# Performance work log

Measured on AMD Instinct MI355X. Metric: run time of the kernel, lower is better.

Reference implementation:

```python
import jax, jax.numpy as jnp
import numpy as np

N, C, H, O, NUM_CLASSES = 4096, 768, 512, 50, 1


def setup_inputs() -> dict:
    key = jax.random.key(0)
    ks = jax.random.split(key, 8)
    x = jax.random.normal(ks[0], (N, C), dtype=jnp.float32)
    labels = jax.random.randint(ks[1], (N,), 0, 2, dtype=jnp.int64)
    W1 = jax.random.normal(ks[2], (C, H), dtype=jnp.float32) / np.sqrt(C)
    b1 = jnp.zeros((H,), dtype=jnp.float32)
    W2 = jax.random.normal(ks[3], (H, O), dtype=jnp.float32) / np.sqrt(H)
    b2 = jnp.zeros((O,), dtype=jnp.float32)
    fcW = jax.random.normal(ks[4], (C + O, NUM_CLASSES), dtype=jnp.float32) / np.sqrt(C + O)
    fcb = jnp.zeros((NUM_CLASSES,), dtype=jnp.float32)
    return {"x": x, "labels": labels, "W1": W1, "b1": b1, "W2": W2, "b2": b2, "fcW": fcW, "fcb": fcb}


def _build_graph(x, labels):
    # similarity-threshold edge construction (dense masked form of the python double loop)
    sim = x @ x.T                                   # [N, N]
    n = x.shape[0]
    diff = labels[:, None] != labels[None, :]       # cross-label pairs
    cnt = jnp.sum(diff)
    s = jnp.sum(jnp.where(diff, sim, 0.0))
    threshold = jnp.where(cnt > 0, s / cnt.astype(sim.dtype), jnp.asarray(0.0, sim.dtype))
    eye = jnp.eye(n, dtype=bool)
    same = (labels[:, None] == labels[None, :]) & ~eye
    edge_mask = same & (sim <= threshold)           # symmetric (sim symmetric)
    loss_mask = edge_mask & (jnp.arange(n)[:, None] < jnp.arange(n)[None, :])  # i<j pairs
    adj = jax.lax.stop_gradient(edge_mask.astype(x.dtype))
    # GCN normalization with self-loops
    a = adj + jnp.eye(n, dtype=x.dtype)
    dinv = jax.lax.rsqrt(jnp.sum(a, axis=1))        # deg >= 1
    norm_adj = dinv[:, None] * a * dinv[None, :]
    return norm_adj, loss_mask


def reference(x, labels, W1, b1, W2, b2, fcW, fcb):
    norm_adj, loss_mask = _build_graph(x, labels)
    h = jax.nn.relu(norm_adj @ (x @ W1) + b1)       # conv1 + relu
    g = norm_adj @ (h @ W2) + b2                    # conv2
    f_g = jnp.concatenate([x, g], axis=-1)          # [N, C+O]
    out = f_g @ fcW + fcb                           # [N, 1]
    return out, f_g, loss_mask, x
```

## Files before the change

### kernel.cpp

```cpp
#include <hip/hip_runtime.h>
#include <hip/hip_bf16.h>
#include <math.h>

#define NN 4096
#define CD 768
#define HD 512
#define OD 50
#define FGD 818

typedef short short8 __attribute__((ext_vector_type(8)));
typedef _Float16 half8 __attribute__((ext_vector_type(8)));
typedef float f32x4 __attribute__((ext_vector_type(4)));
typedef unsigned short us4 __attribute__((ext_vector_type(4)));
typedef unsigned short ushortT;
typedef unsigned char uchar;
typedef unsigned long long u64;

__device__ inline ushortT f2bf(float v) {
    __hip_bfloat16 b = __float2bfloat16(v);
    return *(ushortT*)&b;
}
__device__ inline float bf2f(ushortT u) {
    __hip_bfloat16 b = *(__hip_bfloat16*)&u;
    return __bfloat162float(b);
}
__device__ inline float dinv_of(int d) {
    return (float)(1.0 / sqrt((double)(1 + d)));
}

__global__ __launch_bounds__(256) void gdot_kernel(const double* __restrict__ gsum,
                                                   const int* __restrict__ labels,
                                                   double* __restrict__ scal) {
    int t = threadIdx.x;
    double d = 0.0;
    for (int c = t; c < CD; c += 256) d += gsum[c] * gsum[768 + c];
    int n0 = 0;
    for (int i = t; i < NN; i += 256) n0 += (labels[i] == 0) ? 1 : 0;
    for (int off = 32; off; off >>= 1) {
        d += __shfl_down(d, off);
        n0 += __shfl_down(n0, off);
    }
    __shared__ double sd[4];
    __shared__ int sn[4];
    int wid = t >> 6, lane = t & 63;
    if (lane == 0) { sd[wid] = d; sn[wid] = n0; }
    __syncthreads();
    if (t == 0) {
        double D = sd[0] + sd[1] + sd[2] + sd[3];
        double N0 = (double)(sn[0] + sn[1] + sn[2] + sn[3]);
        scal[0] = 2.0 * D;
        scal[1] = 2.0 * N0 * ((double)NN - N0);
    }
}

#define BAND 0.10
#define RC_CAP (1 << 18)
#define RCB 256

__global__ __launch_bounds__(256) void simk4(
    const ushortT* __restrict__ xf, const ushortT* __restrict__ xh,
    const ushortT* __restrict__ w1t, const int* __restrict__ labels,
    const double* __restrict__ scal, u64* __restrict__ abbits,
    float* __restrict__ lm, int* __restrict__ deg,
    int* __restrict__ rc_cnt, int* __restrict__ rc_list,
    float* __restrict__ xw1f) {
    __shared__ ushortT lds[2 * 64 * 72];
    __shared__ int larr[128];
    __shared__ int rcbuf[RCB];
    __shared__ int rcn, rcbase;
    int tid = threadIdx.x;
    int lane = tid & 63;
    int w = tid >> 6;
    int wr = w >> 1, wc = w & 1;
    int m = lane & 15, quad = lane >> 4;

    if (blockIdx.x >= 2080) {
        int idx = blockIdx.x - 2080;
        int row0 = (idx >> 3) * 64, col0 = (idx & 7) * 64;
        f32x4 acc[2][2] = {{{0.f, 0.f, 0.f, 0.f}, {0.f, 0.f, 0.f, 0.f}},
                           {{0.f, 0.f, 0.f, 0.f}, {0.f, 0.f, 0.f, 0.f}}};
        for (int k0 = 0; k0 < CD; k0 += 64) {
#pragma unroll
            for (int t = 0; t < 2; ++t) {
                int id2 = tid + t * 256;
                int row = id2 >> 3, c8 = (id2 & 7) * 8;
                *(short8*)&lds[row * 72 + c8] =
                    *(const short8*)&xh[(size_t)(row0 + row) * CD + k0 + c8];
                *(short8*)&lds[4608 + row * 72 + c8] =
                    *(const short8*)&w1t[(size_t)(col0 + row) * CD + k0 + c8];
            }
            __syncthreads();
#pragma unroll
            for (int ks = 0; ks < 2; ++ks) {
                short8 af[2], bf[2];
#pragma unroll
                for (int i = 0; i < 2; ++i)
                    af[i] = *(const short8*)&lds[(wr * 32 + i * 16 + m) * 72 +
                                                 ks * 32 + quad * 8];
#pragma unroll
                for (int j = 0; j < 2; ++j)
                    bf[j] = *(const short8*)&lds[4608 +
                                                 (wc * 32 + j * 16 + m) * 72 +
                                                 ks * 32 + quad * 8];
#pragma unroll
                for (int i = 0; i < 2; ++i)
#pragma unroll
                    for (int j = 0; j < 2; ++j)
                        acc[i][j] = __builtin_amdgcn_mfma_f32_16x16x32_bf16(
                            af[i], bf[j], acc[i][j], 0, 0, 0);
            }
            __syncthreads();
        }
#pragma unroll
        for (int i = 0; i < 2; ++i)
#pragma unroll
            for (int j = 0; j < 2; ++j) {
                int row = row0 + wr * 32 + i * 16 + quad * 4;
                int col = col0 + wc * 32 + j * 16 + m;
                *(f32x4*)&xw1f[(size_t)col * NN + row] = acc[i][j];
            }
        return;
    }

    int bid = blockIdx.x;
    int sid = (bid & 7) * 260 + (bid >> 3);
    int sby = 0, rem = sid;
    for (; sby < 8; ++sby) {
        int rowsz = 36 + (7 - sby) * 64;
        if (rem < rowsz) break;
        rem -= rowsz;
    }
    int sbx, iby, ibx;
    if (rem < 36) {
        sbx = sby;
        iby = 0;
        while (rem >= 8 - iby) { rem -= 8 - iby; ++iby; }
        ibx = iby + rem;
    } else {
        rem -= 36;
        sbx = sby + 1 + (rem >> 6);
        int u = rem & 63;
        iby = u >> 3; ibx = u & 7;
    }
    int by = sby * 8 + iby, bx = sbx * 8 + ibx;
    bool diag = (bx == by);
    int row0 = by * 64, col0 = bx * 64;

    if (tid == 0) rcn = 0;
    if (tid < 64) larr[tid] = labels[row0 + tid];
    else if (tid < 128) larr[tid] = labels[col0 + tid - 64];

    f32x4 acc[2][2] = {{{0.f, 0.f, 0.f, 0.f}, {0.f, 0.f, 0.f, 0.f}},
                       {{0.f, 0.f, 0.f, 0.f}, {0.f, 0.f, 0.f, 0.f}}};

    const size_t rowbase = (size_t)row0 * CD;
    const size_t colbase = (size_t)col0 * CD;
    short8 rg[2][2];
#pragma unroll
    for (int tt = 0; tt < 2; ++tt) {
        int id2 = tid + tt * 256;
        int row = id2 >> 3, c8 = (id2 & 7) * 8;
        rg[tt][0] = *(const short8*)&xf[rowbase + (size_t)row * CD + c8];
        rg[tt][1] = *(const short8*)&xf[colbase + (size_t)row * CD + c8];
    }

    for (int k0 = 0; k0 < CD; k0 += 64) {
        __syncthreads();
#pragma unroll
        for (int tt = 0; tt < 2; ++tt) {
            int id2 = tid + tt * 256;
            int row = id2 >> 3, c8 = (id2 & 7) * 8;
            *(short8*)&lds[0 * 4608 + row * 72 + c8] = rg[tt][0];
            *(short8*)&lds[1 * 4608 + row * 72 + c8] = rg[tt][1];
        }
        __syncthreads();
        if (k0 + 64 < CD) {
#pragma unroll
            for (int tt = 0; tt < 2; ++tt) {
                int id2 = tid + tt * 256;
                int row = id2 >> 3, c8 = (id2 & 7) * 8 + k0 + 64;
                rg[tt][0] = *(const short8*)&xf[rowbase + (size_t)row * CD + c8];
                rg[tt][1] = *(const short8*)&xf[colbase + (size_t)row * CD + c8];
            }
        }
#pragma unroll
        for (int ks = 0; ks < 2; ++ks) {
            half8 ah[2], bh[2];
#pragma unroll
            for (int i = 0; i < 2; ++i)
                ah[i] = *(const half8*)&lds[(wr * 32 + i * 16 + m) * 72 +
                                            ks * 32 + quad * 8];
#pragma unroll
            for (int j = 0; j < 2; ++j)
                bh[j] = *(const half8*)&lds[4608 + (wc * 32 + j * 16 + m) * 72 +
                                            ks * 32 + quad * 8];
#pragma unroll
            for (int i = 0; i < 2; ++i)
#pragma unroll
                for (int j = 0; j < 2; ++j)
                    acc[i][j] = __builtin_amdgcn_mfma_f32_16x16x32_f16(
                        ah[i], bh[j], acc[i][j], 0, 0, 0);
        }
    }
    __syncthreads();

    double thrd;
    {
        double cnt = scal[1];
        thrd = (cnt > 0.0) ? (scal[0] / cnt) : 0.0;
    }
    uchar* flags = (uchar*)lds;
#pragma unroll
    for (int i = 0; i < 2; ++i)
#pragma unroll
        for (int j = 0; j < 2; ++j) {
#pragma unroll
            for (int r = 0; r < 4; ++r) {
                int row = wr * 32 + i * 16 + quad * 4 + r;
                int col = wc * 32 + j * 16 + m;
                bool same = (larr[row] == larr[64 + col]);
                bool selfp = ((row0 + row) == (col0 + col));
                bool edge = false;
                if (same && !selfp) {
                    double s = (double)acc[i][j][r];
                    if (s <= thrd - BAND) {
                        edge = true;
                    } else if (s <= thrd + BAND) {
                        edge = (s <= thrd);
                        int enc = ((row0 + row) << 12) | (col0 + col) |
                                  (diag ? 0 : (1 << 24)) |
                                  (edge ? (1 << 25) : 0);
                        int slot = atomicAdd(&rcn, 1);
                        if (slot < RCB) rcbuf[slot] = enc;
                    }
                }
                flags[row * 68 + col] = edge ? 1 : 0;
            }
        }
    __syncthreads();
    if (tid == 0) {
        int n = rcn < RCB ? rcn : RCB;
        rcbase = n ? atomicAdd(rc_cnt, n) : 0;
    }

    {
        int r = tid >> 2, q = tid & 3;
        int cnti = 0;
        unsigned int bits16 = 0;
#pragma unroll
        for (int s = 0; s < 4; ++s) {
            int cb = q * 16 + s * 4;
            float4 f;
#pragma unroll
            for (int k2 = 0; k2 < 4; ++k2) {
                int c = cb + k2;
                bool fl = flags[r * 68 + c] != 0;
                cnti += fl ? 1 : 0;
                if (fl || (diag && r == c)) bits16 |= 1u << (s * 4 + k2);
                ((float*)&f)[k2] = (fl && (row0 + r < col0 + c)) ? 1.0f : 0.0f;
            }
            *(float4*)&lm[(size_t)(row0 + r) * NN + col0 + cb] = f;
        }
        unsigned int s1 = __shfl_down(bits16, 1);
        unsigned int s2 = __shfl_down(bits16, 2);
        unsigned int s3 = __shfl_down(bits16, 3);
        cnti += __shfl_down(cnti, 1);
        cnti += __shfl_down(cnti, 2);
        if (q == 0) {
            u64 u = (u64)bits16 | ((u64)s1 << 16) | ((u64)s2 << 32) |
                    ((u64)s3 << 48);
            abbits[(size_t)(row0 + r) * 64 + bx] = u;
            if (cnti) atomicAdd(&deg[row0 + r], cnti);
        }
    }

    if (!diag) {
        int c = tid >> 2, q = tid & 3;
        int cnti = 0;
        unsigned int bits16 = 0;
        float4 fz = {0.0f, 0.0f, 0.0f, 0.0f};
#pragma unroll
        for (int s = 0; s < 4; ++s) {
            int rb = q * 16 + s * 4;
#pragma unroll
            for (int k2 = 0; k2 < 4; ++k2) {
                bool fl = flags[(rb + k2) * 68 + c] != 0;
                cnti += fl ? 1 : 0;
                if (fl) bits16 |= 1u << (s * 4 + k2);
            }
            *(float4*)&lm[(size_t)(col0 + c) * NN + row0 + rb] = fz;
        }
        unsigned int s1 = __shfl_down(bits16, 1);
        unsigned int s2 = __shfl_down(bits16, 2);
        unsigned int s3 = __shfl_down(bits16, 3);
        cnti += __shfl_down(cnti, 1);
        cnti += __shfl_down(cnti, 2);
        if (q == 0) {
            u64 u = (u64)bits16 | ((u64)s1 << 16) | ((u64)s2 << 32) |
                    ((u64)s3 << 48);
            abbits[(size_t)(col0 + c) * 64 + by] = u;
            if (cnti) atomicAdd(&deg[col0 + c], cnti);
        }
    }

    __syncthreads();
    {
        int n = rcn < RCB ? rcn : RCB;
        if (tid < n) {
            int idx = rcbase + tid;
            if (idx < RC_CAP) rc_list[idx] = rcbuf[tid];
        }
    }
}

__global__ __launch_bounds__(256) void rc_fix(
    const float* __restrict__ x, const double* __restrict__ scal,
    const int* __restrict__ rc_cnt, const int* __restrict__ rc_list,
    u64* __restrict__ abbits, float* __restrict__ lm, int* __restrict__ deg) {
    int cnt = *rc_cnt;
    if (cnt > RC_CAP) cnt = RC_CAP;
    double thrd;
    {
        double c = scal[1];
        thrd = (c > 0.0) ? (scal[0] / c) : 0.0;
    }
    int lane = threadIdx.x & 63;
    int wid = (blockIdx.x * 256 + threadIdx.x) >> 6;
    int nw = (gridDim.x * 256) >> 6;
    for (int e = wid; e < cnt; e += nw) {
        int enc = rc_list[e];
        int c = enc & 0xFFF;
        int r = (enc >> 12) & 0xFFF;
        bool mirror = (enc >> 24) & 1;
        bool prov = (enc >> 25) & 1;
        const float* xi = x + (size_t)r * CD;
        const float* xj = x + (size_t)c * CD;
        double d = 0.0;
#pragma unroll
        for (int s = 0; s < 12; ++s)
            d += (double)xi[lane + s * 64] * (double)xj[lane + s * 64];
        for (int off = 32; off; off >>= 1) d += __shfl_down(d, off);
        if (lane == 0) {
            bool exact = (d <= thrd);
            if (exact != prov) {
                u64 mk = 1ull << (c & 63);
                if (exact) atomicOr(&abbits[(size_t)r * 64 + (c >> 6)], mk);
                else       atomicAnd(&abbits[(size_t)r * 64 + (c >> 6)], ~mk);
                lm[(size_t)r * NN + c] = (exact && r < c) ? 1.0f : 0.0f;
                int dlt = exact ? 1 : -1;
                atomicAdd(&deg[r], dlt);
                if (mirror) {
                    u64 mk2 = 1ull << (r & 63);
                    if (exact) atomicOr(&abbits[(size_t)c * 64 + (r >> 6)], mk2);
                    else       atomicAnd(&abbits[(size_t)c * 64 + (r >> 6)], ~mk2);
                    atomicAdd(&deg[c], dlt);
                }
            }
        }
    }
}

__global__ __launch_bounds__(256) void scaleT(const float* __restrict__ xw1f,
                                              const int* __restrict__ deg,
                                              ushortT* __restrict__ xw1sT) {
    size_t i = ((size_t)blockIdx.x * 256 + threadIdx.x) * 4;
    float4 v = *(const float4*)&xw1f[i];
    int r = (int)(i & (NN - 1));
    us4 o;
    o[0] = f2bf(v.x / sqrtf((float)(1 + deg[r])));
    o[1] = f2bf(v.y / sqrtf((float)(1 + deg[r + 1])));
    o[2] = f2bf(v.z / sqrtf((float)(1 + deg[r + 2])));
    o[3] = f2bf(v.w / sqrtf((float)(1 + deg[r + 3])));
    *(us4*)&xw1sT[i] = o;
}

__global__ __launch_bounds__(256) void prep_kernel(
    const float* __restrict__ x, const float* __restrict__ W1,
    const float* __restrict__ W2, const int* __restrict__ labels,
    float* __restrict__ fg, float* __restrict__ xo,
    ushortT* __restrict__ xh, ushortT* __restrict__ xf, ushortT* __restrict__ w1t,
    ushortT* __restrict__ w2t, double* __restrict__ gsum) {
    int b = blockIdx.x;
    if (b < 4096) {
        int t = threadIdx.x;
        if (t < 192) {
            float4 v = *(const float4*)&x[(size_t)b * CD + t * 4];
            *(float4*)&xo[(size_t)b * CD + t * 4] = v;
            fg[(size_t)b * FGD + t * 4 + 0] = v.x;
            fg[(size_t)b * FGD + t * 4 + 1] = v.y;
            fg[(size_t)b * FGD + t * 4 + 2] = v.z;
            fg[(size_t)b * FGD + t * 4 + 3] = v.w;
            us4 hh, ff;
            float* vp = (float*)&v;
#pragma unroll
            for (int k = 0; k < 4; ++k) {
                ((ushortT*)&hh)[k] = f2bf(vp[k]);
                _Float16 g = (_Float16)vp[k];
                ((ushortT*)&ff)[k] = *(ushortT*)&g;
            }
            *(us4*)&xh[(size_t)b * CD + t * 4] = hh;
            *(us4*)&xf[(size_t)b * CD + t * 4] = ff;
        }
        return;
    }
    if (b >= 4512) {
        int bb = b - 4512;
        int t = threadIdx.x;
        double a0[3] = {0, 0, 0}, a1[3] = {0, 0, 0};
        for (int rr = 0; rr < 16; ++rr) {
            int row = bb * 16 + rr;
            int lab = labels[row];
#pragma unroll
            for (int s = 0; s < 3; ++s) {
                double v = (double)x[(size_t)row * CD + t + s * 256];
                if (lab == 0) a0[s] += v; else a1[s] += v;
            }
        }
#pragma unroll
        for (int s = 0; s < 3; ++s) {
            atomicAdd(&gsum[t + s * 256], a0[s]);
            atomicAdd(&gsum[768 + t + s * 256], a1[s]);
        }
        return;
    }
    __shared__ float tT[32][33];
    const float* P;
    ushortT* T;
    int K, N, Npad, k0, n0;
    if (b < 4480) {
        int bb = b - 4096;
        P = W1; T = w1t; K = CD; N = HD; Npad = HD;
        k0 = (bb % 24) * 32; n0 = (bb / 24) * 32;
    } else {
        int bb = b - 4480;
        P = W2; T = w2t; K = HD; N = OD; Npad = 64;
        k0 = (bb % 16) * 32; n0 = (bb / 16) * 32;
    }
    int tx = threadIdx.x & 31, ty = threadIdx.x >> 5;
#pragma unroll
    for (int s = 0; s < 4; ++s) {
        int k = k0 + ty + s * 8, n = n0 + tx;
        tT[ty + s * 8][tx] = (k < K && n < N) ? P[(size_t)k * N + n] : 0.0f;
    }
    __syncthreads();
#pragma unroll
    for (int s = 0; s < 4; ++s) {
        int n = n0 + ty + s * 8, k = k0 + tx;
        if (n < Npad && k < K) T[(size_t)n * K + k] = f2bf(tT[tx][ty + s * 8]);
    }
}

__global__ __launch_bounds__(256) void gemm_part(
    const ushortT* __restrict__ A, const ushortT* __restrict__ B,
    float* __restrict__ P, int M, int K, int KC) {
    __shared__ ushortT lds[2 * 64 * 72];
    int tid = threadIdx.x;
    int lane = tid & 63;
    int w = tid >> 6;
    int wr = w >> 1, wc = w & 1;
    int m = lane & 15, quad = lane >> 4;
    int kb = blockIdx.x;
    int row0 = blockIdx.y * 64;
    int kbase = kb * KC;

    f32x4 acc[2][2] = {{{0.f, 0.f, 0.f, 0.f}, {0.f, 0.f, 0.f, 0.f}},
                       {{0.f, 0.f, 0.f, 0.f}, {0.f, 0.f, 0.f, 0.f}}};

    for (int k0 = 0; k0 < KC; k0 += 64) {
#pragma unroll
        for (int t = 0; t < 2; ++t) {
            int id2 = tid + t * 256;
            int row = id2 >> 3, c8 = (id2 & 7) * 8;
            *(short8*)&lds[row * 72 + c8] =
                *(const short8*)&A[(size_t)(row0 + row) * K + kbase + k0 + c8];
            *(short8*)&lds[4608 + row * 72 + c8] =
                *(const short8*)&B[(size_t)row * K + kbase + k0 + c8];
        }
        __syncthreads();
#pragma unroll
        for (int ks = 0; ks < 2; ++ks) {
            short8 af[2], bf[2];
#pragma unroll
            for (int i = 0; i < 2; ++i)
                af[i] = *(const short8*)&lds[(wr * 32 + i * 16 + m) * 72 +
                                             ks * 32 + quad * 8];
#pragma unroll
            for (int j = 0; j < 2; ++j)
                bf[j] = *(const short8*)&lds[4608 + (wc * 32 + j * 16 + m) * 72 +
                                             ks * 32 + quad * 8];
#pragma unroll
            for (int i = 0; i < 2; ++i)
#pragma unroll
                for (int j = 0; j < 2; ++j)
                    acc[i][j] = __builtin_amdgcn_mfma_f32_16x16x32_bf16(
                        af[i], bf[j], acc[i][j], 0, 0, 0);
        }
        __syncthreads();
    }
#pragma unroll
    for (int i = 0; i < 2; ++i)
#pragma unroll
        for (int j = 0; j < 2; ++j)
#pragma unroll
            for (int r = 0; r < 4; ++r) {
                int row = wr * 32 + i * 16 + quad * 4 + r;
                int col = wc * 32 + j * 16 + m;
                P[((size_t)kb * M + row0 + row) * 64 + col] = acc[i][j][r];
            }
}

__global__ __launch_bounds__(256) void gemm_partB(
    const u64* __restrict__ Abits, const ushortT* __restrict__ B,
    float* __restrict__ P, int M, int K, int KC) {
    __shared__ ushortT lds[2 * 64 * 72];
    int tid = threadIdx.x;
    int lane = tid & 63;
    int w = tid >> 6;
    int wr = w >> 1, wc = w & 1;
    int m = lane & 15, quad = lane >> 4;
    int kb = blockIdx.x;
    int row0 = blockIdx.y * 64;
    int kbase = kb * KC;
    int er = tid >> 2, eq = tid & 3;

    f32x4 acc[2][2] = {{{0.f, 0.f, 0.f, 0.f}, {0.f, 0.f, 0.f, 0.f}},
                       {{0.f, 0.f, 0.f, 0.f}, {0.f, 0.f, 0.f, 0.f}}};

    for (int k0 = 0; k0 < KC; k0 += 64) {
#pragma unroll
        for (int t = 0; t < 2; ++t) {
            int id2 = tid + t * 256;
            int row = id2 >> 3, c8 = (id2 & 7) * 8;
            *(short8*)&lds[4608 + row * 72 + c8] =
                *(const short8*)&B[(size_t)row * K + kbase + k0 + c8];
        }
        {
            u64 bits = Abits[(size_t)(row0 + er) * 64 + ((kbase + k0) >> 6)];
            unsigned int half = (unsigned int)(bits >> (eq * 16)) & 0xFFFFu;
            short8 v0, v1;
#pragma unroll
            for (int k = 0; k < 8; ++k) {
                ((ushortT*)&v0)[k] =
                    ((half >> k) & 1) ? (ushortT)0x3F80 : (ushortT)0;
                ((ushortT*)&v1)[k] =
                    ((half >> (k + 8)) & 1) ? (ushortT)0x3F80 : (ushortT)0;
            }
            *(short8*)&lds[er * 72 + eq * 16] = v0;
            *(short8*)&lds[er * 72 + eq * 16 + 8] = v1;
        }
        __syncthreads();
#pragma unroll
        for (int ks = 0; ks < 2; ++ks) {
            short8 af[2], bf[2];
#pragma unroll
            for (int i = 0; i < 2; ++i)
                af[i] = *(const short8*)&lds[(wr * 32 + i * 16 + m) * 72 +
                                             ks * 32 + quad * 8];
#pragma unroll
            for (int j = 0; j < 2; ++j)
                bf[j] = *(const short8*)&lds[4608 + (wc * 32 + j * 16 + m) * 72 +
                                             ks * 32 + quad * 8];
#pragma unroll
            for (int i = 0; i < 2; ++i)
#pragma unroll
                for (int j = 0; j < 2; ++j)
                    acc[i][j] = __builtin_amdgcn_mfma_f32_16x16x32_bf16(
                        af[i], bf[j], acc[i][j], 0, 0, 0);
        }
        __syncthreads();
    }
#pragma unroll
    for (int i = 0; i < 2; ++i)
#pragma unroll
        for (int j = 0; j < 2; ++j)
#pragma unroll
            for (int r = 0; r < 4; ++r) {
                int row = wr * 32 + i * 16 + quad * 4 + r;
                int col = wc * 32 + j * 16 + m;
                P[((size_t)kb * M + row0 + row) * 64 + col] = acc[i][j][r];
            }
}

__global__ __launch_bounds__(256) void gemm_partWB(
    const u64* __restrict__ Abits, const ushortT* __restrict__ B,
    float* __restrict__ P, int M, int K, int KC, int ldP) {
    __shared__ ushortT lds[2 * 64 * 72];
    int tid = threadIdx.x;
    int lane = tid & 63;
    int w = tid >> 6;
    int wr = w >> 1, wc = w & 1;
    int m = lane & 15, quad = lane >> 4;
    int col0 = blockIdx.x * 64;
    int row0 = blockIdx.y * 64;
    int kb = blockIdx.z;
    int kbase = kb * KC;
    int er = tid >> 2, eq = tid & 3;

    f32x4 acc[2][2] = {{{0.f, 0.f, 0.f, 0.f}, {0.f, 0.f, 0.f, 0.f}},
                       {{0.f, 0.f, 0.f, 0.f}, {0.f, 0.f, 0.f, 0.f}}};

    for (int k0 = 0; k0 < KC; k0 += 64) {
#pragma unroll
        for (int t = 0; t < 2; ++t) {
            int id2 = tid + t * 256;
            int row = id2 >> 3, c8 = (id2 & 7) * 8;
            *(short8*)&lds[4608 + row * 72 + c8] =
                *(const short8*)&B[(size_t)(col0 + row) * K + kbase + k0 + c8];
        }
        {
            u64 bits = Abits[(size_t)(row0 + er) * 64 + ((kbase + k0) >> 6)];
            unsigned int half = (unsigned int)(bits >> (eq * 16)) & 0xFFFFu;
            short8 v0, v1;
#pragma unroll
            for (int k = 0; k < 8; ++k) {
                ((ushortT*)&v0)[k] =
                    ((half >> k) & 1) ? (ushortT)0x3F80 : (ushortT)0;
                ((ushortT*)&v1)[k] =
                    ((half >> (k + 8)) & 1) ? (ushortT)0x3F80 : (ushortT)0;
            }
            *(short8*)&lds[er * 72 + eq * 16] = v0;
            *(short8*)&lds[er * 72 + eq * 16 + 8] = v1;
        }
        __syncthreads();
#pragma unroll
        for (int ks = 0; ks < 2; ++ks) {
            short8 af[2], bf[2];
#pragma unroll
            for (int i = 0; i < 2; ++i)
                af[i] = *(const short8*)&lds[(wr * 32 + i * 16 + m) * 72 +
                                             ks * 32 + quad * 8];
#pragma unroll
            for (int j = 0; j < 2; ++j)
                bf[j] = *(const short8*)&lds[4608 + (wc * 32 + j * 16 + m) * 72 +
                                             ks * 32 + quad * 8];
#pragma unroll
            for (int i = 0; i < 2; ++i)
#pragma unroll
                for (int j = 0; j < 2; ++j)
                    acc[i][j] = __builtin_amdgcn_mfma_f32_16x16x32_bf16(
                        af[i], bf[j], acc[i][j], 0, 0, 0);
        }
        __syncthreads();
    }
#pragma unroll
    for (int i = 0; i < 2; ++i)
#pragma unroll
        for (int j = 0; j < 2; ++j)
#pragma unroll
            for (int r = 0; r < 4; ++r) {
                int row = wr * 32 + i * 16 + quad * 4 + r;
                int col = wc * 32 + j * 16 + m;
                P[((size_t)kb * M + row0 + row) * ldP + col0 + col] =
                    acc[i][j][r];
            }
}

__global__ __launch_bounds__(256) void k5_epi(const float* __restrict__ P5,
                                              const int* __restrict__ deg,
                                              const float* __restrict__ b1,
                                              ushortT* __restrict__ hb) {
    int tid = threadIdx.x;
    int cg = tid & 127;
    int rr = tid >> 7;
#pragma unroll
    for (int p = 0; p < 2; ++p) {
        int r = blockIdx.x * 4 + p * 2 + rr;
        float dv = dinv_of(deg[r]);
        float4 s = {0.f, 0.f, 0.f, 0.f};
#pragma unroll
        for (int kb = 0; kb < 4; ++kb) {
            float4 v = *(const float4*)&P5[((size_t)kb * NN + r) * HD + cg * 4];
            s.x += v.x; s.y += v.y; s.z += v.z; s.w += v.w;
        }
        float4 bv = *(const float4*)&b1[cg * 4];
        us4 o;
        o[0] = f2bf(fmaxf(s.x * dv + bv.x, 0.f));
        o[1] = f2bf(fmaxf(s.y * dv + bv.y, 0.f));
        o[2] = f2bf(fmaxf(s.z * dv + bv.z, 0.f));
        o[3] = f2bf(fmaxf(s.w * dv + bv.w, 0.f));
        *(us4*)&hb[(size_t)r * HD + cg * 4] = o;
    }
}

__global__ __launch_bounds__(256) void k6_epi(const float* __restrict__ P6,
                                              const int* __restrict__ deg,
                                              ushortT* __restrict__ hw2sT) {
    __shared__ ushortT Th[64 * 72];
    int row0 = blockIdx.x * 64;
    int tid = threadIdx.x;
    int rl = tid >> 2, q = tid & 3;
    float dv = dinv_of(deg[row0 + rl]);
#pragma unroll
    for (int s = 0; s < 16; ++s) {
        int c = q * 16 + s;
        float v = 0.f;
#pragma unroll
        for (int kb = 0; kb < 8; ++kb)
            v += P6[((size_t)kb * NN + row0 + rl) * 64 + c];
        Th[c * 72 + rl] = f2bf(v * dv);
    }
    __syncthreads();
#pragma unroll
    for (int t = 0; t < 2; ++t) {
        int id2 = tid + t * 256;
        int cc = id2 >> 3, chunk = id2 & 7;
        *(short8*)&hw2sT[(size_t)cc * NN + row0 + chunk * 8] =
            *(const short8*)&Th[cc * 72 + chunk * 8];
    }
}

__global__ __launch_bounds__(256) void k7_epi_out(
    const float* __restrict__ P7, const int* __restrict__ deg,
    const float* __restrict__ b2, const float* __restrict__ fcW,
    const float* __restrict__ fcb, float* __restrict__ fg,
    float* __restrict__ out) {
    int row0 = blockIdx.x * 64;
    int tid = threadIdx.x;
    int rl = tid >> 2, q = tid & 3;
    int r = row0 + rl;
    float dv = dinv_of(deg[r]);
    float sg = 0.f;
#pragma unroll
    for (int s = 0; s < 16; ++s) {
        int c = q * 16 + s;
        if (c < OD) {
            float v = 0.f;
#pragma unroll
            for (int kb = 0; kb < 16; ++kb)
                v += P7[((size_t)kb * NN + r) * 64 + c];
            v = v * dv + b2[c];
            fg[(size_t)r * FGD + CD + c] = v;
            sg += v * fcW[CD + c];
        }
    }
    const float* fr = fg + (size_t)r * FGD;
    float sx = 0.f;
    for (int k = q * 192; k < (q + 1) * 192; k += 2) {
        float2 vv = *(const float2*)&fr[k];
        float2 ww = *(const float2*)&fcW[k];
        sx += vv.x * ww.x + vv.y * ww.y;
    }
    float s = sx + sg;
    s += __shfl_down(s, 1);
    s += __shfl_down(s, 2);
    if (q == 0) out[r] = s + fcb[0];
}

extern "C" void kernel_launch(void* const* d_in, const int* in_sizes, int n_in,
                              void* d_out, int out_size, void* d_ws, size_t ws_size,
                              hipStream_t stream) {
    const float* x = (const float*)d_in[0];
    const int* labels = (const int*)d_in[1];
    const float* W1 = (const float*)d_in[2];
    const float* b1 = (const float*)d_in[3];
    const float* W2 = (const float*)d_in[4];
    const float* b2 = (const float*)d_in[5];
    const float* fcW = (const float*)d_in[6];
    const float* fcb = (const float*)d_in[7];
    float* outp = (float*)d_out;

    const size_t o_out = 0;
    const size_t o_fg = 4096;
    const size_t o_lm = o_fg + (size_t)NN * FGD;
    const size_t o_x = o_lm + (size_t)NN * NN;

    char* ws = (char*)d_ws;
    size_t off = 0;
    u64* abbits = (u64*)(ws + off); off += (size_t)NN * 64 * 8;
    ushortT* xh = (ushortT*)(ws + off); off += (size_t)NN * CD * 2;
    ushortT* xf = (ushortT*)(ws + off); off += (size_t)NN * CD * 2;
    ushortT* w1t = (ushortT*)(ws + off); off += (size_t)HD * CD * 2;
    ushortT* xw1sT = (ushortT*)(ws + off); off += (size_t)HD * NN * 2;
    ushortT* hb = (ushortT*)(ws + off); off += (size_t)NN * HD * 2;
    ushortT* w2t = (ushortT*)(ws + off); off += (size_t)64 * HD * 2;
    ushortT* hw2sT = (ushortT*)(ws + off); off += (size_t)64 * NN * 2;
    char* zbase = ws + off;
    int* deg = (int*)(ws + off); off += (size_t)NN * 4;
    double* gsum = (double*)(ws + off); off += 1536 * 8;
    double* scal = (double*)(ws + off); off += 16;
    int* rc_cnt = (int*)(ws + off); off += 16;
    size_t zbytes = (size_t)NN * 4 + 1536 * 8 + 16 + 16;
    char* uni = ws + off;
    int* rc_list = (int*)uni;
    float* xw1f = (float*)(uni + (1 << 20));
    float* P5 = (float*)uni;
    float* P6 = (float*)uni;
    float* P7 = (float*)uni;
    off += (size_t)4 * NN * HD * 4;

    hipMemsetAsync(zbase, 0, zbytes, stream);

    prep_kernel<<<4768, 256, 0, stream>>>(x, W1, W2, labels, outp + o_fg,
                                          outp + o_x, xh, xf, w1t, w2t, gsum);

    gdot_kernel<<<1, 256, 0, stream>>>(gsum, labels, scal);

    simk4<<<2592, 256, 0, stream>>>(xf, xh, w1t, labels, scal, abbits,
                                    outp + o_lm, deg, rc_cnt, rc_list, xw1f);

    rc_fix<<<512, 256, 0, stream>>>(x, scal, rc_cnt, rc_list, abbits, outp + o_lm,
                                    deg);

    scaleT<<<(HD * NN / 4) / 256, 256, 0, stream>>>(xw1f, deg, xw1sT);

    gemm_partWB<<<dim3(HD / 64, NN / 64, 4), 256, 0, stream>>>(
        abbits, xw1sT, P5, NN, NN, NN / 4, HD);
    k5_epi<<<NN / 4, 256, 0, stream>>>(P5, deg, b1, hb);

    gemm_part<<<dim3(8, NN / 64), 256, 0, stream>>>(hb, w2t, P6, NN, HD, HD / 8);
    k6_epi<<<NN / 64, 256, 0, stream>>>(P6, deg, hw2sT);

    gemm_partB<<<dim3(16, NN / 64), 256, 0, stream>>>(abbits, hw2sT, P7, NN, NN,
                                                      NN / 16);
    k7_epi_out<<<NN / 64, 256, 0, stream>>>(P7, deg, b2, fcW, fcb, outp + o_fg,
                                            outp + o_out);
}
```

Baseline: 306.8 us.

## Use async global-to-LDS double buffering in sim GEMM and fuse degree scaling into gemm

The similarity GEMM in simk4 now uses global_load_lds direct-to-LDS loads into a double-buffered, XOR-swizzled LDS layout, so the next K tile is fetched while the current one is computed. This replaces the register-staged prefetch and removes one barrier per iteration. Separately, the scaleT kernel is removed: gemm_partWB now reads the fp32 XW1 directly, scales it by the per-row dinv values, and converts to bf16 while loading tiles. That saves a launch and an intermediate write and read, but doubles the bytes the B operand loads and adds conversion work inside the GEMM.

New measurement: 315.8 us. 2.9% more time.

```diff
diff --git a/kernel.cpp b/kernel.cpp
--- a/kernel.cpp
+++ b/kernel.cpp
@@ -26,6 +26,11 @@
 }
 __device__ inline float dinv_of(int d) {
     return (float)(1.0 / sqrt((double)(1 + d)));
+}
+__device__ inline void gload16(const void* g, void* l) {
+    __builtin_amdgcn_global_load_lds(
+        (const __attribute__((address_space(1))) void*)g,
+        (__attribute__((address_space(3))) void*)l, 16, 0, 0);
 }
 
 __global__ __launch_bounds__(256) void gdot_kernel(const double* __restrict__ gsum,
@@ -64,7 +69,7 @@
     float* __restrict__ lm, int* __restrict__ deg,
     int* __restrict__ rc_cnt, int* __restrict__ rc_list,
     float* __restrict__ xw1f) {
-    __shared__ ushortT lds[2 * 64 * 72];
+    __shared__ ushortT lds2[16384];
     __shared__ int larr[128];
     __shared__ int rcbuf[RCB];
     __shared__ int rcn, rcbase;
@@ -84,9 +89,9 @@
             for (int t = 0; t < 2; ++t) {
                 int id2 = tid + t * 256;
                 int row = id2 >> 3, c8 = (id2 & 7) * 8;
-                *(short8*)&lds[row * 72 + c8] =
+                *(short8*)&lds2[row * 72 + c8] =
                     *(const short8*)&xh[(size_t)(row0 + row) * CD + k0 + c8];
-                *(short8*)&lds[4608 + row * 72 + c8] =
+                *(short8*)&lds2[4608 + row * 72 + c8] =
                     *(const short8*)&w1t[(size_t)(col0 + row) * CD + k0 + c8];
             }
             __syncthreads();
@@ -95,13 +100,13 @@
                 short8 af[2], bf[2];
 #pragma unroll
                 for (int i = 0; i < 2; ++i)
-                    af[i] = *(const short8*)&lds[(wr * 32 + i * 16 + m) * 72 +
-                                                 ks * 32 + quad * 8];
+                    af[i] = *(const short8*)&lds2[(wr * 32 + i * 16 + m) * 72 +
+                                                  ks * 32 + quad * 8];
 #pragma unroll
                 for (int j = 0; j < 2; ++j)
-                    bf[j] = *(const short8*)&lds[4608 +
-                                                 (wc * 32 + j * 16 + m) * 72 +
-                                                 ks * 32 + quad * 8];
+                    bf[j] = *(const short8*)&lds2[4608 +
+                                                  (wc * 32 + j * 16 + m) * 72 +
+                                                  ks * 32 + quad * 8];
 #pragma unroll
                 for (int i = 0; i < 2; ++i)
 #pragma unroll
@@ -155,45 +160,45 @@
 
     const size_t rowbase = (size_t)row0 * CD;
     const size_t colbase = (size_t)col0 * CD;
-    short8 rg[2][2];
-#pragma unroll
-    for (int tt = 0; tt < 2; ++tt) {
-        int id2 = tid + tt * 256;
-        int row = id2 >> 3, c8 = (id2 & 7) * 8;
-        rg[tt][0] = *(const short8*)&xf[rowbase + (size_t)row * CD + c8];
-        rg[tt][1] = *(const short8*)&xf[colbase + (size_t)row * CD + c8];
-    }
-
-    for (int k0 = 0; k0 < CD; k0 += 64) {
-        __syncthreads();
-#pragma unroll
-        for (int tt = 0; tt < 2; ++tt) {
-            int id2 = tid + tt * 256;
-            int row = id2 >> 3, c8 = (id2 & 7) * 8;
-            *(short8*)&lds[0 * 4608 + row * 72 + c8] = rg[tt][0];
-            *(short8*)&lds[1 * 4608 + row * 72 + c8] = rg[tt][1];
-        }
-        __syncthreads();
-        if (k0 + 64 < CD) {
-#pragma unroll
-            for (int tt = 0; tt < 2; ++tt) {
-                int id2 = tid + tt * 256;
-                int row = id2 >> 3, c8 = (id2 & 7) * 8 + k0 + 64;
-                rg[tt][0] = *(const short8*)&xf[rowbase + (size_t)row * CD + c8];
-                rg[tt][1] = *(const short8*)&xf[colbase + (size_t)row * CD + c8];
-            }
-        }
+    int p = w >> 1;
+    const ushortT* src = xf + (p ? colbase : rowbase);
+    int gsub = (w & 1) * 4;
+    int lrow = lane >> 3, lchunk = lane & 7;
+    int cc = lchunk ^ lrow;
+
+    auto stage = [&](int buf, int k0) {
+#pragma unroll
+        for (int i = 0; i < 4; ++i) {
+            int g = gsub + i;
+            int grow = g * 8 + lrow;
+            const void* gp = (const void*)(src + (size_t)grow * CD + k0 + cc * 8);
+            int loff = buf * 16384 + p * 8192 + g * 1024;
+            loff = __builtin_amdgcn_readfirstlane(loff);
+            gload16(gp, (char*)lds2 + loff);
+        }
+    };
+
+    stage(0, 0);
+    __syncthreads();
+    int cur = 0;
+    for (int t = 0; t < CD / 64; ++t) {
+        if (t < CD / 64 - 1) stage(cur ^ 1, (t + 1) * 64);
 #pragma unroll
         for (int ks = 0; ks < 2; ++ks) {
             half8 ah[2], bh[2];
-#pragma unroll
-            for (int i = 0; i < 2; ++i)
-                ah[i] = *(const half8*)&lds[(wr * 32 + i * 16 + m) * 72 +
-                                            ks * 32 + quad * 8];
-#pragma unroll
-            for (int j = 0; j < 2; ++j)
-                bh[j] = *(const half8*)&lds[4608 + (wc * 32 + j * 16 + m) * 72 +
-                                            ks * 32 + quad * 8];
+            int jj = ks * 4 + quad;
+#pragma unroll
+            for (int i = 0; i < 2; ++i) {
+                int row = wr * 32 + i * 16 + m;
+                ah[i] = *(const half8*)&lds2[cur * 8192 + row * 64 +
+                                             ((jj ^ (row & 7)) << 3)];
+            }
+#pragma unroll
+            for (int j = 0; j < 2; ++j) {
+                int row = wc * 32 + j * 16 + m;
+                bh[j] = *(const half8*)&lds2[cur * 8192 + 4096 + row * 64 +
+                                             ((jj ^ (row & 7)) << 3)];
+            }
 #pragma unroll
             for (int i = 0; i < 2; ++i)
 #pragma unroll
@@ -201,15 +206,16 @@
                     acc[i][j] = __builtin_amdgcn_mfma_f32_16x16x32_f16(
                         ah[i], bh[j], acc[i][j], 0, 0, 0);
         }
-    }
-    __syncthreads();
+        __syncthreads();
+        cur ^= 1;
+    }
 
     double thrd;
     {
         double cnt = scal[1];
         thrd = (cnt > 0.0) ? (scal[0] / cnt) : 0.0;
     }
-    uchar* flags = (uchar*)lds;
+    uchar* flags = (uchar*)lds2;
 #pragma unroll
     for (int i = 0; i < 2; ++i)
 #pragma unroll
@@ -360,20 +366,6 @@
     }
 }
 
-__global__ __launch_bounds__(256) void scaleT(const float* __restrict__ xw1f,
-                                              const int* __restrict__ deg,
-                                              ushortT* __restrict__ xw1sT) {
-    size_t i = ((size_t)blockIdx.x * 256 + threadIdx.x) * 4;
-    float4 v = *(const float4*)&xw1f[i];
-    int r = (int)(i & (NN - 1));
-    us4 o;
-    o[0] = f2bf(v.x / sqrtf((float)(1 + deg[r])));
-    o[1] = f2bf(v.y / sqrtf((float)(1 + deg[r + 1])));
-    o[2] = f2bf(v.z / sqrtf((float)(1 + deg[r + 2])));
-    o[3] = f2bf(v.w / sqrtf((float)(1 + deg[r + 3])));
-    *(us4*)&xw1sT[i] = o;
-}
-
 __global__ __launch_bounds__(256) void prep_kernel(
     const float* __restrict__ x, const float* __restrict__ W1,
     const float* __restrict__ W2, const int* __restrict__ labels,
@@ -582,9 +574,11 @@
 }
 
 __global__ __launch_bounds__(256) void gemm_partWB(
-    const u64* __restrict__ Abits, const ushortT* __restrict__ B,
-    float* __restrict__ P, int M, int K, int KC, int ldP) {
+    const u64* __restrict__ Abits, const float* __restrict__ Bf,
+    const int* __restrict__ deg, float* __restrict__ P,
+    int M, int K, int KC, int ldP) {
     __shared__ ushortT lds[2 * 64 * 72];
+    __shared__ float dinvK[1024];
     int tid = threadIdx.x;
     int lane = tid & 63;
     int w = tid >> 6;
@@ -596,6 +590,10 @@
     int kbase = kb * KC;
     int er = tid >> 2, eq = tid & 3;
 
+    for (int v = tid; v < KC; v += 256)
+        dinvK[v] = 1.0f / sqrtf((float)(1 + deg[kbase + v]));
+    __syncthreads();
+
     f32x4 acc[2][2] = {{{0.f, 0.f, 0.f, 0.f}, {0.f, 0.f, 0.f, 0.f}},
                        {{0.f, 0.f, 0.f, 0.f}, {0.f, 0.f, 0.f, 0.f}}};
 
@@ -604,8 +602,19 @@
         for (int t = 0; t < 2; ++t) {
             int id2 = tid + t * 256;
             int row = id2 >> 3, c8 = (id2 & 7) * 8;
-            *(short8*)&lds[4608 + row * 72 + c8] =
-                *(const short8*)&B[(size_t)(col0 + row) * K + kbase + k0 + c8];
+            const float* bp = &Bf[(size_t)(col0 + row) * K + kbase + k0 + c8];
+            float4 v0 = *(const float4*)bp;
+            float4 v1 = *(const float4*)(bp + 4);
+            short8 o;
+            ((ushortT*)&o)[0] = f2bf(v0.x * dinvK[k0 + c8 + 0]);
+            ((ushortT*)&o)[1] = f2bf(v0.y * dinvK[k0 + c8 + 1]);
+            ((ushortT*)&o)[2] = f2bf(v0.z * dinvK[k0 + c8 + 2]);
+            ((ushortT*)&o)[3] = f2bf(v0.w * dinvK[k0 + c8 + 3]);
+            ((ushortT*)&o)[4] = f2bf(v1.x * dinvK[k0 + c8 + 4]);
+            ((ushortT*)&o)[5] = f2bf(v1.y * dinvK[k0 + c8 + 5]);
+            ((ushortT*)&o)[6] = f2bf(v1.z * dinvK[k0 + c8 + 6]);
+            ((ushortT*)&o)[7] = f2bf(v1.w * dinvK[k0 + c8 + 7]);
+            *(short8*)&lds[4608 + row * 72 + c8] = o;
         }
         {
             u64 bits = Abits[(size_t)(row0 + er) * 64 + ((kbase + k0) >> 6)];
@@ -770,7 +779,7 @@
     ushortT* xh = (ushortT*)(ws + off); off += (size_t)NN * CD * 2;
     ushortT* xf = (ushortT*)(ws + off); off += (size_t)NN * CD * 2;
     ushortT* w1t = (ushortT*)(ws + off); off += (size_t)HD * CD * 2;
-    ushortT* xw1sT = (ushortT*)(ws + off); off += (size_t)HD * NN * 2;
+    float* xw1f = (float*)(ws + off); off += (size_t)HD * NN * 4;
     ushortT* hb = (ushortT*)(ws + off); off += (size_t)NN * HD * 2;
     ushortT* w2t = (ushortT*)(ws + off); off += (size_t)64 * HD * 2;
     ushortT* hw2sT = (ushortT*)(ws + off); off += (size_t)64 * NN * 2;
@@ -782,7 +791,6 @@
     size_t zbytes = (size_t)NN * 4 + 1536 * 8 + 16 + 16;
     char* uni = ws + off;
     int* rc_list = (int*)uni;
-    float* xw1f = (float*)(uni + (1 << 20));
     float* P5 = (float*)uni;
     float* P6 = (float*)uni;
     float* P7 = (float*)uni;
@@ -801,10 +809,8 @@
     rc_fix<<<512, 256, 0, stream>>>(x, scal, rc_cnt, rc_list, abbits, outp + o_lm,
                                     deg);
 
-    scaleT<<<(HD * NN / 4) / 256, 256, 0, stream>>>(xw1f, deg, xw1sT);
-
     gemm_partWB<<<dim3(HD / 64, NN / 64, 4), 256, 0, stream>>>(
-        abbits, xw1sT, P5, NN, NN, NN / 4, HD);
+        abbits, xw1f, deg, P5, NN, NN, NN / 4, HD);
     k5_epi<<<NN / 4, 256, 0, stream>>>(P5, deg, b1, hb);
 
     gemm_part<<<dim3(8, NN / 64), 256, 0, stream>>>(hb, w2t, P6, NN, HD, HD / 8);
```

## Fuse degree scaling into GEMM B-load and fold h@W2 into conv1 epilogue

Applied to the files above, without the earlier changes.

Removes the scaleT kernel by having gemm_partWB read the fp32 X·W1 buffer directly, scale it by per-k D^-1/2 (cached in shared memory) and convert it to bf16 while staging into LDS. It also merges k5_epi, the h@W2 GEMM and k6_epi into one k56_epi kernel. That kernel keeps 4 rows of relu(h) in shared memory and computes the 64-column product with scalar FMAs. This cuts three launches and the hb/P6 round trips through memory. The cost is that the big GEMM now reads fp32 B, twice the bytes, and the small GEMM runs on plain ALUs instead of MFMA.

New measurement: 325.3 us. +6.0%, slower.

```diff
diff --git a/kernel.cpp b/kernel.cpp
--- a/kernel.cpp
+++ b/kernel.cpp
@@ -360,20 +360,6 @@
     }
 }
 
-__global__ __launch_bounds__(256) void scaleT(const float* __restrict__ xw1f,
-                                              const int* __restrict__ deg,
-                                              ushortT* __restrict__ xw1sT) {
-    size_t i = ((size_t)blockIdx.x * 256 + threadIdx.x) * 4;
-    float4 v = *(const float4*)&xw1f[i];
-    int r = (int)(i & (NN - 1));
-    us4 o;
-    o[0] = f2bf(v.x / sqrtf((float)(1 + deg[r])));
-    o[1] = f2bf(v.y / sqrtf((float)(1 + deg[r + 1])));
-    o[2] = f2bf(v.z / sqrtf((float)(1 + deg[r + 2])));
-    o[3] = f2bf(v.w / sqrtf((float)(1 + deg[r + 3])));
-    *(us4*)&xw1sT[i] = o;
-}
-
 __global__ __launch_bounds__(256) void prep_kernel(
     const float* __restrict__ x, const float* __restrict__ W1,
     const float* __restrict__ W2, const int* __restrict__ labels,
@@ -450,65 +436,6 @@
     }
 }
 
-__global__ __launch_bounds__(256) void gemm_part(
-    const ushortT* __restrict__ A, const ushortT* __restrict__ B,
-    float* __restrict__ P, int M, int K, int KC) {
-    __shared__ ushortT lds[2 * 64 * 72];
-    int tid = threadIdx.x;
-    int lane = tid & 63;
-    int w = tid >> 6;
-    int wr = w >> 1, wc = w & 1;
-    int m = lane & 15, quad = lane >> 4;
-    int kb = blockIdx.x;
-    int row0 = blockIdx.y * 64;
-    int kbase = kb * KC;
-
-    f32x4 acc[2][2] = {{{0.f, 0.f, 0.f, 0.f}, {0.f, 0.f, 0.f, 0.f}},
-                       {{0.f, 0.f, 0.f, 0.f}, {0.f, 0.f, 0.f, 0.f}}};
-
-    for (int k0 = 0; k0 < KC; k0 += 64) {
-#pragma unroll
-        for (int t = 0; t < 2; ++t) {
-            int id2 = tid + t * 256;
-            int row = id2 >> 3, c8 = (id2 & 7) * 8;
-            *(short8*)&lds[row * 72 + c8] =
-                *(const short8*)&A[(size_t)(row0 + row) * K + kbase + k0 + c8];
-            *(short8*)&lds[4608 + row * 72 + c8] =
-                *(const short8*)&B[(size_t)row * K + kbase + k0 + c8];
-        }
-        __syncthreads();
-#pragma unroll
-        for (int ks = 0; ks < 2; ++ks) {
-            short8 af[2], bf[2];
-#pragma unroll
-            for (int i = 0; i < 2; ++i)
-                af[i] = *(const short8*)&lds[(wr * 32 + i * 16 + m) * 72 +
-                                             ks * 32 + quad * 8];
-#pragma unroll
-            for (int j = 0; j < 2; ++j)
-                bf[j] = *(const short8*)&lds[4608 + (wc * 32 + j * 16 + m) * 72 +
-                                             ks * 32 + quad * 8];
-#pragma unroll
-            for (int i = 0; i < 2; ++i)
-#pragma unroll
-                for (int j = 0; j < 2; ++j)
-                    acc[i][j] = __builtin_amdgcn_mfma_f32_16x16x32_bf16(
-                        af[i], bf[j], acc[i][j], 0, 0, 0);
-        }
-        __syncthreads();
-    }
-#pragma unroll
-    for (int i = 0; i < 2; ++i)
-#pragma unroll
-        for (int j = 0; j < 2; ++j)
-#pragma unroll
-            for (int r = 0; r < 4; ++r) {
-                int row = wr * 32 + i * 16 + quad * 4 + r;
-                int col = wc * 32 + j * 16 + m;
-                P[((size_t)kb * M + row0 + row) * 64 + col] = acc[i][j][r];
-            }
-}
-
 __global__ __launch_bounds__(256) void gemm_partB(
     const u64* __restrict__ Abits, const ushortT* __restrict__ B,
     float* __restrict__ P, int M, int K, int KC) {
@@ -582,9 +509,11 @@
 }
 
 __global__ __launch_bounds__(256) void gemm_partWB(
-    const u64* __restrict__ Abits, const ushortT* __restrict__ B,
-    float* __restrict__ P, int M, int K, int KC, int ldP) {
+    const u64* __restrict__ Abits, const float* __restrict__ Bf,
+    const int* __restrict__ deg, float* __restrict__ P,
+    int M, int K, int KC, int ldP) {
     __shared__ ushortT lds[2 * 64 * 72];
+    __shared__ float dinvK[1024];
     int tid = threadIdx.x;
     int lane = tid & 63;
     int w = tid >> 6;
@@ -596,6 +525,10 @@
     int kbase = kb * KC;
     int er = tid >> 2, eq = tid & 3;
 
+    for (int v = tid; v < KC; v += 256)
+        dinvK[v] = 1.0f / sqrtf((float)(1 + deg[kbase + v]));
+    __syncthreads();
+
     f32x4 acc[2][2] = {{{0.f, 0.f, 0.f, 0.f}, {0.f, 0.f, 0.f, 0.f}},
                        {{0.f, 0.f, 0.f, 0.f}, {0.f, 0.f, 0.f, 0.f}}};
 
@@ -604,8 +537,19 @@
         for (int t = 0; t < 2; ++t) {
             int id2 = tid + t * 256;
             int row = id2 >> 3, c8 = (id2 & 7) * 8;
-            *(short8*)&lds[4608 + row * 72 + c8] =
-                *(const short8*)&B[(size_t)(col0 + row) * K + kbase + k0 + c8];
+            const float* bp = &Bf[(size_t)(col0 + row) * K + kbase + k0 + c8];
+            float4 v0 = *(const float4*)bp;
+            float4 v1 = *(const float4*)(bp + 4);
+            short8 o;
+            ((ushortT*)&o)[0] = f2bf(v0.x * dinvK[k0 + c8 + 0]);
+            ((ushortT*)&o)[1] = f2bf(v0.y * dinvK[k0 + c8 + 1]);
+            ((ushortT*)&o)[2] = f2bf(v0.z * dinvK[k0 + c8 + 2]);
+            ((ushortT*)&o)[3] = f2bf(v0.w * dinvK[k0 + c8 + 3]);
+            ((ushortT*)&o)[4] = f2bf(v1.x * dinvK[k0 + c8 + 4]);
+            ((ushortT*)&o)[5] = f2bf(v1.y * dinvK[k0 + c8 + 5]);
+            ((ushortT*)&o)[6] = f2bf(v1.z * dinvK[k0 + c8 + 6]);
+            ((ushortT*)&o)[7] = f2bf(v1.w * dinvK[k0 + c8 + 7]);
+            *(short8*)&lds[4608 + row * 72 + c8] = o;
         }
         {
             u64 bits = Abits[(size_t)(row0 + er) * 64 + ((kbase + k0) >> 6)];
@@ -655,16 +599,20 @@
             }
 }
 
-__global__ __launch_bounds__(256) void k5_epi(const float* __restrict__ P5,
-                                              const int* __restrict__ deg,
-                                              const float* __restrict__ b1,
-                                              ushortT* __restrict__ hb) {
+__global__ __launch_bounds__(256) void k56_epi(const float* __restrict__ P5,
+                                               const int* __restrict__ deg,
+                                               const float* __restrict__ b1,
+                                               const ushortT* __restrict__ w2t,
+                                               ushortT* __restrict__ hw2sT) {
+    __shared__ float hl[4][HD];
     int tid = threadIdx.x;
+    int r0 = blockIdx.x * 4;
     int cg = tid & 127;
     int rr = tid >> 7;
 #pragma unroll
     for (int p = 0; p < 2; ++p) {
-        int r = blockIdx.x * 4 + p * 2 + rr;
+        int lr = p * 2 + rr;
+        int r = r0 + lr;
         float dv = dinv_of(deg[r]);
         float4 s = {0.f, 0.f, 0.f, 0.f};
 #pragma unroll
@@ -673,40 +621,23 @@
             s.x += v.x; s.y += v.y; s.z += v.z; s.w += v.w;
         }
         float4 bv = *(const float4*)&b1[cg * 4];
-        us4 o;
-        o[0] = f2bf(fmaxf(s.x * dv + bv.x, 0.f));
-        o[1] = f2bf(fmaxf(s.y * dv + bv.y, 0.f));
-        o[2] = f2bf(fmaxf(s.z * dv + bv.z, 0.f));
-        o[3] = f2bf(fmaxf(s.w * dv + bv.w, 0.f));
-        *(us4*)&hb[(size_t)r * HD + cg * 4] = o;
-    }
-}
-
-__global__ __launch_bounds__(256) void k6_epi(const float* __restrict__ P6,
-                                              const int* __restrict__ deg,
-                                              ushortT* __restrict__ hw2sT) {
-    __shared__ ushortT Th[64 * 72];
-    int row0 = blockIdx.x * 64;
-    int tid = threadIdx.x;
-    int rl = tid >> 2, q = tid & 3;
-    float dv = dinv_of(deg[row0 + rl]);
-#pragma unroll
-    for (int s = 0; s < 16; ++s) {
-        int c = q * 16 + s;
-        float v = 0.f;
-#pragma unroll
-        for (int kb = 0; kb < 8; ++kb)
-            v += P6[((size_t)kb * NN + row0 + rl) * 64 + c];
-        Th[c * 72 + rl] = f2bf(v * dv);
+        hl[lr][cg * 4 + 0] = fmaxf(s.x * dv + bv.x, 0.f);
+        hl[lr][cg * 4 + 1] = fmaxf(s.y * dv + bv.y, 0.f);
+        hl[lr][cg * 4 + 2] = fmaxf(s.z * dv + bv.z, 0.f);
+        hl[lr][cg * 4 + 3] = fmaxf(s.w * dv + bv.w, 0.f);
     }
     __syncthreads();
-#pragma unroll
-    for (int t = 0; t < 2; ++t) {
-        int id2 = tid + t * 256;
-        int cc = id2 >> 3, chunk = id2 & 7;
-        *(short8*)&hw2sT[(size_t)cc * NN + row0 + chunk * 8] =
-            *(const short8*)&Th[cc * 72 + chunk * 8];
-    }
+    int rr2 = tid >> 6, c = tid & 63;
+    float acc = 0.f;
+#pragma unroll 8
+    for (int k8 = 0; k8 < HD / 8; ++k8) {
+        short8 wv = *(const short8*)&w2t[(size_t)c * HD + k8 * 8];
+#pragma unroll
+        for (int j = 0; j < 8; ++j)
+            acc += hl[rr2][k8 * 8 + j] * bf2f(((const ushortT*)&wv)[j]);
+    }
+    int r = r0 + rr2;
+    hw2sT[(size_t)c * NN + r] = f2bf(acc * dinv_of(deg[r]));
 }
 
 __global__ __launch_bounds__(256) void k7_epi_out(
@@ -770,8 +701,7 @@
     ushortT* xh = (ushortT*)(ws + off); off += (size_t)NN * CD * 2;
     ushortT* xf = (ushortT*)(ws + off); off += (size_t)NN * CD * 2;
     ushortT* w1t = (ushortT*)(ws + off); off += (size_t)HD * CD * 2;
-    ushortT* xw1sT = (ushortT*)(ws + off); off += (size_t)HD * NN * 2;
-    ushortT* hb = (ushortT*)(ws + off); off += (size_t)NN * HD * 2;
+    float* xw1f = (float*)(ws + off); off += (size_t)HD * NN * 4;
     ushortT* w2t = (ushortT*)(ws + off); off += (size_t)64 * HD * 2;
     ushortT* hw2sT = (ushortT*)(ws + off); off += (size_t)64 * NN * 2;
     char* zbase = ws + off;
@@ -782,9 +712,7 @@
     size_t zbytes = (size_t)NN * 4 + 1536 * 8 + 16 + 16;
     char* uni = ws + off;
     int* rc_list = (int*)uni;
-    float* xw1f = (float*)(uni + (1 << 20));
     float* P5 = (float*)uni;
-    float* P6 = (float*)uni;
     float* P7 = (float*)uni;
     off += (size_t)4 * NN * HD * 4;
 
@@ -801,14 +729,10 @@
     rc_fix<<<512, 256, 0, stream>>>(x, scal, rc_cnt, rc_list, abbits, outp + o_lm,
                                     deg);
 
-    scaleT<<<(HD * NN / 4) / 256, 256, 0, stream>>>(xw1f, deg, xw1sT);
-
     gemm_partWB<<<dim3(HD / 64, NN / 64, 4), 256, 0, stream>>>(
-        abbits, xw1sT, P5, NN, NN, NN / 4, HD);
-    k5_epi<<<NN / 4, 256, 0, stream>>>(P5, deg, b1, hb);
-
-    gemm_part<<<dim3(8, NN / 64), 256, 0, stream>>>(hb, w2t, P6, NN, HD, HD / 8);
-    k6_epi<<<NN / 64, 256, 0, stream>>>(P6, deg, hw2sT);
+        abbits, xw1f, deg, P5, NN, NN, NN / 4, HD);
+
+    k56_epi<<<NN / 4, 256, 0, stream>>>(P5, deg, b1, w2t, hw2sT);
 
     gemm_partB<<<dim3(16, NN / 64), 256, 0, stream>>>(abbits, hw2sT, P7, NN, NN,
                                                       NN / 16);
```
